# Performance work log

Hardware: AMD Instinct MI355X
Metric: run time of the kernel (lower is better)

Reference implementation:

```python
import jax, jax.numpy as jnp
import numpy as np

N = 100000   # nodes
E = 800000   # edges (avg degree 8)
H = 96       # hidden_features from ALIGNNConfig
LN_EPS = 1e-5


def _layernorm(x, g, b):
    mu = jnp.mean(x, axis=-1, keepdims=True)
    var = jnp.mean(jnp.square(x - mu), axis=-1, keepdims=True)
    return (x - mu) * jax.lax.rsqrt(var + LN_EPS) * g + b


def setup_inputs() -> dict:
    key = jax.random.key(0)
    ks = jax.random.split(key, 24)
    s = 1.0 / np.sqrt(H)  # torch nn.Linear default init scale
    w = lambda k: jax.random.uniform(k, (H, H), jnp.float32, -s, s)
    b = lambda k: jax.random.uniform(k, (H,), jnp.float32, -s, s)
    return {
        "node_feats": jax.random.normal(ks[0], (N, H), jnp.float32),
        "edge_feats": jax.random.normal(ks[1], (E, H), jnp.float32),
        "time_feats": jax.random.normal(ks[2], (1, H), jnp.float32),
        "src": jax.random.randint(ks[3], (E,), 0, N, jnp.int32),
        "dst": jax.random.randint(ks[4], (E,), 0, N, jnp.int32),
        "W_tp": w(ks[5]), "b_tp": b(ks[6]),
        "W_sg": w(ks[7]), "b_sg": b(ks[8]),
        "W_dg": w(ks[9]), "b_dg": b(ks[10]),
        "W_eg": w(ks[11]), "b_eg": b(ks[12]),
        "W_su": w(ks[13]), "b_su": b(ks[14]),
        "W_du": w(ks[15]), "b_du": b(ks[16]),
        "g_ln_e": jnp.ones((H,), jnp.float32), "b_ln_e": jnp.zeros((H,), jnp.float32),
        "g_ln_n": jnp.ones((H,), jnp.float32), "b_ln_n": jnp.zeros((H,), jnp.float32),
    }


def reference(node_feats, edge_feats, time_feats, src, dst,
              W_tp, b_tp, W_sg, b_sg, W_dg, b_dg, W_eg, b_eg,
              W_su, b_su, W_du, b_du,
              g_ln_e, b_ln_e, g_ln_n, b_ln_n):
    n = node_feats.shape[0]
    tp = time_feats @ W_tp + b_tp                       # [1,H], broadcasts over nodes
    e_src = node_feats @ W_sg + b_sg + tp               # [N,H]
    e_dst = node_feats @ W_dg + b_dg                    # [N,H]
    # apply_edges(u_add_v) + edge_gate
    m = e_src[src] + e_dst[dst] + (edge_feats @ W_eg + b_eg)   # [E,H]
    sigma = jax.nn.sigmoid(m)
    Bh = node_feats @ W_du + b_du                       # [N,H]
    # update_all(u_mul_e, sum) and update_all(copy_e, sum): scatter-sum to dst
    sum_sigma_h = jax.ops.segment_sum(Bh[src] * sigma, dst, num_segments=n)
    sum_sigma = jax.ops.segment_sum(sigma, dst, num_segments=n)
    h = sum_sigma_h / (sum_sigma + 1e-6)
    x = node_feats @ W_su + b_su + h
    x = jax.nn.silu(_layernorm(x, g_ln_n, b_ln_n))
    y = jax.nn.silu(_layernorm(m, g_ln_e, b_ln_e))
    # residual
    x = node_feats + x
    y = edge_feats + y
    return (x, y)
```

## Files before the change

### kernel.cpp

```cpp
#include <hip/hip_runtime.h>
#include <hip/hip_bf16.h>
#include <math.h>

#define HF 96

typedef __attribute__((ext_vector_type(8))) short bf16x8;
typedef __attribute__((ext_vector_type(4))) float f32x4;

__device__ __forceinline__ short f2b(float x) {
    __hip_bfloat16 h = __float2bfloat16(x);
    return *reinterpret_cast<short*>(&h);
}
__device__ __forceinline__ float b2f(short s) {
    __hip_bfloat16 h = *reinterpret_cast<__hip_bfloat16*>(&s);
    return __bfloat162float(h);
}

__global__ void k_prep(const float* __restrict__ Weg, const float* __restrict__ Wsg,
                       const float* __restrict__ Wdg, const float* __restrict__ Wdu,
                       const float* __restrict__ Wsu,
                       const float* __restrict__ timef, const float* __restrict__ Wtp,
                       const float* __restrict__ btp,
                       const float* __restrict__ bsg, const float* __restrict__ bdg,
                       const float* __restrict__ bdu, const float* __restrict__ bsu,
                       short* __restrict__ WegT, short* __restrict__ WT4,
                       float* __restrict__ bias4) {
    int c = threadIdx.x;
    int k = blockIdx.x;
    if (c >= HF) return;
    if (k < HF) {
        WegT[c * HF + k]           = f2b(Weg[k * HF + c]);
        WT4[(0 * HF + c) * HF + k] = f2b(Wsg[k * HF + c]);
        WT4[(1 * HF + c) * HF + k] = f2b(Wdg[k * HF + c]);
        WT4[(2 * HF + c) * HF + k] = f2b(Wdu[k * HF + c]);
        WT4[(3 * HF + c) * HF + k] = f2b(Wsu[k * HF + c]);
    } else {
        float acc = btp[c];
#pragma unroll 8
        for (int kk = 0; kk < HF; ++kk) acc = fmaf(timef[kk], Wtp[kk * HF + c], acc);
        bias4[0 * HF + c] = bsg[c] + acc;
        bias4[1 * HF + c] = bdg[c];
        bias4[2 * HF + c] = bdu[c];
        bias4[3 * HF + c] = bsu[c];
    }
}

__global__ void k_hist(const int* __restrict__ dst, unsigned* __restrict__ counts, int E) {
    int e = blockIdx.x * 256 + threadIdx.x;
    if (e < E) atomicAdd(&counts[dst[e]], 1u);
}

__global__ __launch_bounds__(256)
void k_scanA(const unsigned* __restrict__ counts, unsigned* __restrict__ bsum, int n) {
    int b = blockIdx.x, t = threadIdx.x;
    int base = b * 512;
    unsigned s = 0;
    int i0 = base + t, i1 = base + 256 + t;
    if (i0 < n) s += counts[i0];
    if (i1 < n) s += counts[i1];
    __shared__ unsigned ls[256];
    ls[t] = s; __syncthreads();
    for (int off = 128; off > 0; off >>= 1) {
        if (t < off) ls[t] += ls[t + off];
        __syncthreads();
    }
    if (t == 0) bsum[b] = ls[0];
}

__global__ __launch_bounds__(512)
void k_scanC(const unsigned* __restrict__ counts, const unsigned* __restrict__ bsum,
             unsigned* __restrict__ offs, unsigned* __restrict__ cursor, int n) {
    int b = blockIdx.x, t = threadIdx.x;
    __shared__ unsigned ls[512];
    __shared__ unsigned boffS;

    unsigned s0 = 0;
    for (int i = t; i < b; i += 512) s0 += bsum[i];
    ls[t] = s0; __syncthreads();
    for (int off = 256; off > 0; off >>= 1) {
        if (t < off) ls[t] += ls[t + off];
        __syncthreads();
    }
    if (t == 0) boffS = ls[0];
    __syncthreads();
    unsigned boffv = boffS;
    __syncthreads();

    int i = b * 512 + t;
    unsigned v = (i < n) ? counts[i] : 0u;
    ls[t] = v; __syncthreads();
#pragma unroll
    for (int off = 1; off < 512; off <<= 1) {
        unsigned u = (t >= off) ? ls[t - off] : 0u;
        __syncthreads();
        ls[t] += u;
        __syncthreads();
    }
    unsigned excl = ls[t] - v + boffv;
    if (i < n) { offs[i] = excl; cursor[i] = excl; }
    if (i == n - 1) offs[n] = excl + v;
}

__global__ void k_scatter(const int* __restrict__ src, const int* __restrict__ dst,
                          unsigned* __restrict__ cursor,
                          unsigned* __restrict__ slot_of, int* __restrict__ srcs_slot,
                          int E) {
    int e = blockIdx.x * 256 + threadIdx.x;
    if (e < E) {
        int d = dst[e];
        unsigned pos = atomicAdd(&cursor[d], 1u);
        slot_of[e] = pos;
        srcs_slot[pos] = src[e];
    }
}

__device__ __forceinline__ void load_afrag(const float* __restrict__ ap, bf16x8* a) {
#pragma unroll
    for (int kt = 0; kt < 3; ++kt) {
        float4 f0 = *(const float4*)(ap + kt * 32);
        float4 f1 = *(const float4*)(ap + kt * 32 + 4);
        bf16x8 fr;
        fr[0] = f2b(f0.x); fr[1] = f2b(f0.y); fr[2] = f2b(f0.z); fr[3] = f2b(f0.w);
        fr[4] = f2b(f1.x); fr[5] = f2b(f1.y); fr[6] = f2b(f1.z); fr[7] = f2b(f1.w);
        a[kt] = fr;
    }
}

__global__ __launch_bounds__(256)
void k_node_mfma(const float* __restrict__ nf,
                 const short* __restrict__ WT4,
                 const float* __restrict__ bias4,
                 short* __restrict__ esrc16, short* __restrict__ edstA16,
                 short* __restrict__ bh16, float* __restrict__ xlin, int n) {
    int wid = threadIdx.x >> 6;
    int lane = threadIdx.x & 63;
    int lr = lane & 15, lg = lane >> 4;
    int nbase = blockIdx.x * 64 + wid * 16;

    bf16x8 a[3];
    {
        int arow = nbase + lr; if (arow > n - 1) arow = n - 1;
        load_afrag(nf + (size_t)arow * HF + lg * 8, a);
    }

#pragma unroll
    for (int w = 0; w < 4; ++w) {
#pragma unroll
        for (int tn = 0; tn < 6; ++tn) {
            f32x4 acc = {0.f, 0.f, 0.f, 0.f};
            int feat = tn * 16 + lr;
            size_t boff = (size_t)(w * HF + feat) * HF + lg * 8;
#pragma unroll
            for (int kt = 0; kt < 3; ++kt) {
                bf16x8 bfr = *(const bf16x8*)(WT4 + boff + kt * 32);
                acc = __builtin_amdgcn_mfma_f32_16x16x32_bf16(a[kt], bfr, acc, 0, 0, 0);
            }
            float bias = bias4[w * HF + feat];
#pragma unroll
            for (int r = 0; r < 4; ++r) {
                int node = nbase + lg * 4 + r;
                if (node < n) {
                    float v = acc[r] + bias;
                    size_t o = (size_t)node * HF + feat;
                    if (w == 0)      esrc16[o]  = f2b(v);
                    else if (w == 1) edstA16[o] = f2b(v);
                    else if (w == 2) bh16[o]    = f2b(v);
                    else             xlin[o]    = v;
                }
            }
        }
    }
}

__global__ __launch_bounds__(256, 4)
void k_edge_mfma(const float* __restrict__ ef, const int* __restrict__ src,
                 const int* __restrict__ dst, const unsigned* __restrict__ slot_of,
                 const short* __restrict__ WegT,
                 const float* __restrict__ beg,
                 const short* __restrict__ esrc16, const short* __restrict__ edstA16,
                 const float* __restrict__ g_ln, const float* __restrict__ b_ln,
                 unsigned char* __restrict__ sq,
                 float* __restrict__ y, int E) {
    int wid = threadIdx.x >> 6;
    int lane = threadIdx.x & 63;
    int lr = lane & 15, lg = lane >> 4;
    int ebase = blockIdx.x * 64 + wid * 16;

    __shared__ float redS[4][4][64];
    __shared__ float redQ[4][4][64];

    int e_r[4], s_r[4], d_r[4], sl_r[4];
    bool val[4];
#pragma unroll
    for (int r = 0; r < 4; ++r) {
        e_r[r] = ebase + lg * 4 + r;
        val[r] = (e_r[r] < E);
        int ec = val[r] ? e_r[r] : E - 1;
        s_r[r] = src[ec];
        d_r[r] = dst[ec];
        sl_r[r] = (int)slot_of[ec];
    }

    unsigned short esb[6][4], edb[6][4];
#pragma unroll
    for (int tn = 0; tn < 6; ++tn) {
        int feat = tn * 16 + lr;
#pragma unroll
        for (int r = 0; r < 4; ++r) {
            esb[tn][r] = *(const unsigned short*)&esrc16[(size_t)s_r[r] * HF + feat];
            edb[tn][r] = *(const unsigned short*)&edstA16[(size_t)d_r[r] * HF + feat];
        }
    }

    bf16x8 a[3];
    {
        int arow = ebase + lr; if (arow > E - 1) arow = E - 1;
        load_afrag(ef + (size_t)arow * HF + lg * 8, a);
    }

    f32x4 acc[6];
    __builtin_amdgcn_s_setprio(1);
#pragma unroll
    for (int tn = 0; tn < 6; ++tn) {
        acc[tn] = (f32x4){0.f, 0.f, 0.f, 0.f};
        size_t boff = (size_t)(tn * 16 + lr) * HF + lg * 8;
#pragma unroll
        for (int kt = 0; kt < 3; ++kt) {
            bf16x8 bfr = *(const bf16x8*)(WegT + boff + kt * 32);
            acc[tn] = __builtin_amdgcn_mfma_f32_16x16x32_bf16(a[kt], bfr, acc[tn], 0, 0, 0);
        }
    }
    __builtin_amdgcn_s_setprio(0);

    float psum[4] = {0.f, 0.f, 0.f, 0.f}, psq[4] = {0.f, 0.f, 0.f, 0.f};
#pragma unroll
    for (int tn = 0; tn < 6; ++tn) {
        int feat = tn * 16 + lr;
        float bg = beg[feat];
#pragma unroll
        for (int r = 0; r < 4; ++r) {
            float v = acc[tn][r] + bg
                    + b2f((short)esb[tn][r]) + b2f((short)edb[tn][r]);
            acc[tn][r] = v;
            psum[r] += v;
            psq[r]  += v * v;
            if (val[r]) {
                float sg = 1.0f / (1.0f + __expf(-v));
                int q = __float2int_rn(sg * 255.0f);
                if (q < 1) q = 1;
                sq[(size_t)sl_r[r] * HF + feat] = (unsigned char)q;
            }
        }
    }

#pragma unroll
    for (int r = 0; r < 4; ++r) {
        redS[wid][r][lg * 16 + lr] = psum[r];
        redQ[wid][r][lg * 16 + lr] = psq[r];
    }
    float mean[4], rstd[4];
#pragma unroll
    for (int r = 0; r < 4; ++r) {
        const float4* ps4 = (const float4*)&redS[wid][r][0];
        const float4* pq4 = (const float4*)&redQ[wid][r][0];
        float s = 0.f, q = 0.f;
#pragma unroll
        for (int i = 0; i < 4; ++i) {
            float4 aa = ps4[lg * 4 + i];
            float4 bb = pq4[lg * 4 + i];
            s += (aa.x + aa.y) + (aa.z + aa.w);
            q += (bb.x + bb.y) + (bb.z + bb.w);
        }
        mean[r] = s * (1.0f / HF);
        float var = q * (1.0f / HF) - mean[r] * mean[r];
        rstd[r] = rsqrtf(var + 1e-5f);
    }

#pragma unroll
    for (int tn = 0; tn < 6; ++tn) {
        int feat = tn * 16 + lr;
        float g = g_ln[feat], bb = b_ln[feat];
#pragma unroll
        for (int r = 0; r < 4; ++r) {
            if (!val[r]) continue;
            float v = acc[tn][r];
            float ln = (v - mean[r]) * rstd[r] * g + bb;
            float si = ln / (1.0f + __expf(-ln));
            size_t oe = (size_t)e_r[r] * HF + feat;
            __builtin_nontemporal_store(ef[oe] + si, &y[oe]);
        }
    }
}

__global__ void k_node_fin(const float* __restrict__ nf,
                           const unsigned* __restrict__ offs,
                           const int* __restrict__ srcs_slot,
                           const unsigned char* __restrict__ sq,
                           const short* __restrict__ bh16,
                           const float* __restrict__ g_ln, const float* __restrict__ b_ln,
                           float* __restrict__ x, int n) {
    int j = threadIdx.x;
    int ty = threadIdx.y;
    int node = blockIdx.x * 4 + ty;
    bool valid = (node < n);

    float xv = 0.0f;
    if (valid) {
        unsigned st = offs[node], en = offs[node + 1];
        unsigned den = 0;
        long long num = 0;
        unsigned d = st;
        while (d < en) {
            unsigned cnt = en - d; if (cnt > 8u) cnt = 8u;
            int sarr[8]; unsigned qarr[8];
#pragma unroll
            for (int i = 0; i < 8; ++i) {
                if ((unsigned)i < cnt) {
                    sarr[i] = srcs_slot[d + i];
                    qarr[i] = sq[(size_t)(d + i) * HF + j];
                }
            }
            int barr[8];
#pragma unroll
            for (int i = 0; i < 8; ++i) {
                if ((unsigned)i < cnt)
                    barr[i] = __float2int_rn(b2f(bh16[(size_t)sarr[i] * HF + j]) * 4096.0f);
            }
#pragma unroll
            for (int i = 0; i < 8; ++i) {
                if ((unsigned)i < cnt) {
                    den += qarr[i];
                    num += (long long)(int)qarr[i] * (long long)barr[i];
                }
            }
            d += cnt;
        }
        float ssv  = (float)den * (1.0f / 255.0f);
        float sshv = (float)num * (1.0f / (255.0f * 4096.0f));
        float h = sshv / (ssv + 1e-6f);
        size_t o = (size_t)node * HF + j;
        xv = x[o] + h;
    }

    __shared__ float reds[4][HF];
    __shared__ float redq[4][HF];
    reds[ty][j] = xv;
    redq[ty][j] = xv * xv;
    __syncthreads();
    if (j < 48) { reds[ty][j] += reds[ty][j + 48]; redq[ty][j] += redq[ty][j + 48]; } __syncthreads();
    if (j < 24) { reds[ty][j] += reds[ty][j + 24]; redq[ty][j] += redq[ty][j + 24]; } __syncthreads();
    if (j < 12) { reds[ty][j] += reds[ty][j + 12]; redq[ty][j] += redq[ty][j + 12]; } __syncthreads();
    if (j < 6)  { reds[ty][j] += reds[ty][j + 6];  redq[ty][j] += redq[ty][j + 6];  } __syncthreads();
    if (j < 3)  { reds[ty][j] += reds[ty][j + 3];  redq[ty][j] += redq[ty][j + 3];  } __syncthreads();

    if (valid) {
        float sum = reds[ty][0] + reds[ty][1] + reds[ty][2];
        float sqv = redq[ty][0] + redq[ty][1] + redq[ty][2];
        float mean = sum * (1.0f / HF);
        float var  = sqv * (1.0f / HF) - mean * mean;
        float lnv  = (xv - mean) * rsqrtf(var + 1e-5f) * g_ln[j] + b_ln[j];
        float silu = lnv / (1.0f + __expf(-lnv));
        size_t o = (size_t)node * HF + j;
        x[o] = nf[o] + silu;
    }
}

extern "C" void kernel_launch(void* const* d_in, const int* in_sizes, int n_in,
                              void* d_out, int out_size, void* d_ws, size_t ws_size,
                              hipStream_t stream) {
    const float* node_feats = (const float*)d_in[0];
    const float* edge_feats = (const float*)d_in[1];
    const float* time_feats = (const float*)d_in[2];
    const int*   src        = (const int*)d_in[3];
    const int*   dst        = (const int*)d_in[4];
    const float* W_tp = (const float*)d_in[5];  const float* b_tp = (const float*)d_in[6];
    const float* W_sg = (const float*)d_in[7];  const float* b_sg = (const float*)d_in[8];
    const float* W_dg = (const float*)d_in[9];  const float* b_dg = (const float*)d_in[10];
    const float* W_eg = (const float*)d_in[11]; const float* b_eg = (const float*)d_in[12];
    const float* W_su = (const float*)d_in[13]; const float* b_su = (const float*)d_in[14];
    const float* W_du = (const float*)d_in[15]; const float* b_du = (const float*)d_in[16];
    const float* g_ln_e = (const float*)d_in[17]; const float* b_ln_e = (const float*)d_in[18];
    const float* g_ln_n = (const float*)d_in[19]; const float* b_ln_n = (const float*)d_in[20];

    int n = in_sizes[0] / HF;
    int e = in_sizes[1] / HF;

    float* ws    = (float*)d_ws;
    float* bias4 = ws;
    short* WegT  = (short*)(ws + 384);
    short* WT4   = (short*)(ws + 384 + 4608);
    short* esrc16  = (short*)(ws + 384 + 4608 + 18432);
    short* edstA16 = esrc16  + (size_t)n * HF;
    short* bh16    = edstA16 + (size_t)n * HF;
    unsigned char* sq = (unsigned char*)(bh16 + (size_t)n * HF);
    unsigned* slot_of = (unsigned*)(sq + (size_t)e * HF);
    int* srcs_slot    = (int*)(slot_of + (size_t)e);
    unsigned* offs    = (unsigned*)(srcs_slot + (size_t)e);
    unsigned* cursor  = offs + (size_t)(n + 1);
    unsigned* counts  = cursor + (size_t)n;
    unsigned* bsum    = counts + (size_t)n;

    float* x = (float*)d_out;
    float* y = x + (size_t)n * HF;

    int nb = (n + 511) / 512;

    hipMemsetAsync(counts, 0, (size_t)n * sizeof(unsigned), stream);

    k_prep<<<HF + 1, HF, 0, stream>>>(W_eg, W_sg, W_dg, W_du, W_su,
                                      time_feats, W_tp, b_tp,
                                      b_sg, b_dg, b_du, b_su,
                                      WegT, WT4, bias4);

    k_hist<<<(e + 255) / 256, 256, 0, stream>>>(dst, counts, e);
    k_scanA<<<nb, 256, 0, stream>>>(counts, bsum, n);
    k_scanC<<<nb, 512, 0, stream>>>(counts, bsum, offs, cursor, n);
    k_scatter<<<(e + 255) / 256, 256, 0, stream>>>(src, dst, cursor, slot_of, srcs_slot, e);

    k_node_mfma<<<(n + 63) / 64, 256, 0, stream>>>(node_feats, WT4, bias4,
                                                   esrc16, edstA16, bh16, x, n);

    k_edge_mfma<<<(e + 63) / 64, 256, 0, stream>>>(edge_feats, src, dst, slot_of,
                                                   WegT, b_eg,
                                                   esrc16, edstA16,
                                                   g_ln_e, b_ln_e,
                                                   sq, y, e);

    dim3 b2(HF, 4);
    k_node_fin<<<(n + 3) / 4, b2, 0, stream>>>(node_feats, offs, srcs_slot,
                                               sq, bh16,
                                               g_ln_n, b_ln_n, x, n);
}
```

Measured before the change: 684.4 us.

## Split each node's incoming edges across four thread rows in node finalize

The node finalize kernel now uses one block per node, and its four thread rows take interleaved incoming edges and accumulate partial sums. The partials are then reduced through shared memory before the layernorm. This is meant to shorten the serial gather chain per thread and expose more memory parallelism across a node's neighbors. In exchange it launches four times as many blocks, leaves three of four rows idle during the reduction and layernorm, and drops the unrolled batched loads.

Result: slower. 800.1 us (+16.9%).

```diff
diff --git a/kernel.cpp b/kernel.cpp
--- a/kernel.cpp
+++ b/kernel.cpp
@@ -292,70 +292,58 @@
     }
 }
 
-__global__ void k_node_fin(const float* __restrict__ nf,
-                           const unsigned* __restrict__ offs,
-                           const int* __restrict__ srcs_slot,
-                           const unsigned char* __restrict__ sq,
-                           const short* __restrict__ bh16,
-                           const float* __restrict__ g_ln, const float* __restrict__ b_ln,
-                           float* __restrict__ x, int n) {
+__global__ __launch_bounds__(384)
+void k_node_fin(const float* __restrict__ nf,
+                const unsigned* __restrict__ offs,
+                const int* __restrict__ srcs_slot,
+                const unsigned char* __restrict__ sq,
+                const short* __restrict__ bh16,
+                const float* __restrict__ g_ln, const float* __restrict__ b_ln,
+                float* __restrict__ x, int n) {
     int j = threadIdx.x;
     int ty = threadIdx.y;
-    int node = blockIdx.x * 4 + ty;
-    bool valid = (node < n);
+    int node = blockIdx.x;
+
+    unsigned st = offs[node], en = offs[node + 1];
+    unsigned den = 0;
+    long long num = 0;
+    for (unsigned d = st + ty; d < en; d += 4) {
+        unsigned q = sq[(size_t)d * HF + j];
+        int s = srcs_slot[d];
+        int bhi = __float2int_rn(b2f(bh16[(size_t)s * HF + j]) * 4096.0f);
+        den += q;
+        num += (long long)(int)q * (long long)bhi;
+    }
+
+    __shared__ unsigned  denS[4][HF];
+    __shared__ long long numS[4][HF];
+    __shared__ float reds[HF], redq[HF];
+    denS[ty][j] = den;
+    numS[ty][j] = num;
+    __syncthreads();
 
     float xv = 0.0f;
-    if (valid) {
-        unsigned st = offs[node], en = offs[node + 1];
-        unsigned den = 0;
-        long long num = 0;
-        unsigned d = st;
-        while (d < en) {
-            unsigned cnt = en - d; if (cnt > 8u) cnt = 8u;
-            int sarr[8]; unsigned qarr[8];
-#pragma unroll
-            for (int i = 0; i < 8; ++i) {
-                if ((unsigned)i < cnt) {
-                    sarr[i] = srcs_slot[d + i];
-                    qarr[i] = sq[(size_t)(d + i) * HF + j];
-                }
-            }
-            int barr[8];
-#pragma unroll
-            for (int i = 0; i < 8; ++i) {
-                if ((unsigned)i < cnt)
-                    barr[i] = __float2int_rn(b2f(bh16[(size_t)sarr[i] * HF + j]) * 4096.0f);
-            }
-#pragma unroll
-            for (int i = 0; i < 8; ++i) {
-                if ((unsigned)i < cnt) {
-                    den += qarr[i];
-                    num += (long long)(int)qarr[i] * (long long)barr[i];
-                }
-            }
-            d += cnt;
-        }
-        float ssv  = (float)den * (1.0f / 255.0f);
-        float sshv = (float)num * (1.0f / (255.0f * 4096.0f));
+    if (ty == 0) {
+        unsigned  dt = denS[0][j] + denS[1][j] + denS[2][j] + denS[3][j];
+        long long nt = numS[0][j] + numS[1][j] + numS[2][j] + numS[3][j];
+        float ssv  = (float)dt * (1.0f / 255.0f);
+        float sshv = (float)nt * (1.0f / (255.0f * 4096.0f));
         float h = sshv / (ssv + 1e-6f);
         size_t o = (size_t)node * HF + j;
         xv = x[o] + h;
-    }
-
-    __shared__ float reds[4][HF];
-    __shared__ float redq[4][HF];
-    reds[ty][j] = xv;
-    redq[ty][j] = xv * xv;
+        reds[j] = xv;
+        redq[j] = xv * xv;
+    }
     __syncthreads();
-    if (j < 48) { reds[ty][j] += reds[ty][j + 48]; redq[ty][j] += redq[ty][j + 48]; } __syncthreads();
-    if (j < 24) { reds[ty][j] += reds[ty][j + 24]; redq[ty][j] += redq[ty][j + 24]; } __syncthreads();
-    if (j < 12) { reds[ty][j] += reds[ty][j + 12]; redq[ty][j] += redq[ty][j + 12]; } __syncthreads();
-    if (j < 6)  { reds[ty][j] += reds[ty][j + 6];  redq[ty][j] += redq[ty][j + 6];  } __syncthreads();
-    if (j < 3)  { reds[ty][j] += reds[ty][j + 3];  redq[ty][j] += redq[ty][j + 3];  } __syncthreads();
-
-    if (valid) {
-        float sum = reds[ty][0] + reds[ty][1] + reds[ty][2];
-        float sqv = redq[ty][0] + redq[ty][1] + redq[ty][2];
+    if (ty == 0 && j < 48) { reds[j] += reds[j + 48]; redq[j] += redq[j + 48]; } __syncthreads();
+    if (ty == 0 && j < 24) { reds[j] += reds[j + 24]; redq[j] += redq[j + 24]; } __syncthreads();
+    if (ty == 0 && j < 12) { reds[j] += reds[j + 12]; redq[j] += redq[j + 12]; } __syncthreads();
+    if (ty == 0 && j < 6)  { reds[j] += reds[j + 6];  redq[j] += redq[j + 6];  } __syncthreads();
+    if (ty == 0 && j < 3)  { reds[j] += reds[j + 3];  redq[j] += redq[j + 3];  } __syncthreads();
+
+    if (ty == 0) {
+        float sum = reds[0] + reds[1] + reds[2];
+        float sqv = redq[0] + redq[1] + redq[2];
         float mean = sum * (1.0f / HF);
         float var  = sqv * (1.0f / HF) - mean * mean;
         float lnv  = (xv - mean) * rsqrtf(var + 1e-5f) * g_ln[j] + b_ln[j];
@@ -427,7 +415,7 @@
                                                    sq, y, e);
 
     dim3 b2(HF, 4);
-    k_node_fin<<<(n + 3) / 4, b2, 0, stream>>>(node_feats, offs, srcs_slot,
-                                               sq, bh16,
-                                               g_ln_n, b_ln_n, x, n);
-}
+    k_node_fin<<<n, b2, 0, stream>>>(node_feats, offs, srcs_slot,
+                                     sq, bh16,
+                                     g_ln_n, b_ln_n, x, n);
+}
```
